# Optimization experiments

Hardware: AMD Instinct MI355X
Metric: run time of the kernel (lower is better)

## Reference

```python
import jax, jax.numpy as jnp
import numpy as np

N_NODES = 100000
N_EDGES = 1600000
D_FEAT = 32


def setup_inputs() -> dict:
    key = jax.random.key(0)
    k1, k2, k3, k4, k5 = jax.random.split(key, 5)
    src_feats = jax.random.normal(k1, (N_NODES, D_FEAT), dtype=jnp.float32)
    cj = jax.random.uniform(k2, (N_NODES, 1), dtype=jnp.float32)
    ci = jax.random.uniform(k3, (N_NODES, 1), dtype=jnp.float32)
    src_idx = jax.random.randint(k4, (N_EDGES,), 0, N_NODES, dtype=jnp.int32)
    dst_idx = jax.random.randint(k5, (N_EDGES,), 0, N_NODES, dtype=jnp.int32)
    return {"src_feats": src_feats, "cj": cj, "ci": ci,
            "src_idx": src_idx, "dst_idx": dst_idx}


def reference(src_feats, cj, ci, src_idx, dst_idx):
    # Dropout in eval mode (identity). Training-mode dropout is stochastic and
    # excluded from the correctness baseline.
    weighted = src_feats * cj                      # [N, d] scale by src norm coeff
    msgs = weighted[src_idx]                       # [E, d] gather (copy_u)
    agg = jax.ops.segment_sum(msgs, dst_idx, num_segments=N_NODES)  # [N, d] sum aggregate
    return agg * ci                                # [N, d] scale by dst norm coeff
```

## Files before the change

### kernel.cpp

```cpp
#include <hip/hip_runtime.h>
#include <hip/hip_fp16.h>

#define N_NODES 100000
#define N_EDGES 1600000
#define D_FEAT 32
#define CAP 32
#define NXCD 8
#define NODES_PER_XCD (N_NODES / NXCD)
#define EDGE_THREADS (N_EDGES / 4)
#define EDGE_BLOCKS ((EDGE_THREADS + 255) / 256)

typedef int   __attribute__((ext_vector_type(4))) i32x4;
typedef float __attribute__((ext_vector_type(4))) f32x4;

__global__ __launch_bounds__(256) void lgc_weight(
    const f32x4* __restrict__ feats4,
    const float* __restrict__ cj,
    __half2*     __restrict__ w2)
{
    int tid = blockIdx.x * 256 + threadIdx.x;
    float c = cj[tid >> 3];
    f32x4 v = __builtin_nontemporal_load(&feats4[tid]);
    __half2 h0 = __floats2half2_rn(v.x * c, v.y * c);
    __half2 h1 = __floats2half2_rn(v.z * c, v.w * c);
    w2[tid * 2 + 0] = h0;
    w2[tid * 2 + 1] = h1;
}

__global__ __launch_bounds__(256) void lgc_bucket(
    const i32x4*  __restrict__ dst4,
    const i32x4*  __restrict__ src4,
    const __half* __restrict__ weighted,
    int*          __restrict__ cnt,
    int*          __restrict__ bucket,
    float*        __restrict__ out)
{
    int x  = blockIdx.x % NXCD;
    int lb = blockIdx.x / NXCD;
    int t  = lb * 256 + threadIdx.x;
    if (t >= EDGE_THREADS) return;

    const int lo = x * NODES_PER_XCD;
    const int hi = lo + NODES_PER_XCD;

    i32x4 d4 = __builtin_nontemporal_load(&dst4[t]);
    bool ix = (d4.x >= lo) & (d4.x < hi);
    bool iy = (d4.y >= lo) & (d4.y < hi);
    bool iz = (d4.z >= lo) & (d4.z < hi);
    bool iw = (d4.w >= lo) & (d4.w < hi);
    if (!(ix | iy | iz | iw)) return;

    i32x4 s4 = __builtin_nontemporal_load(&src4[t]);
    int ds[4] = {d4.x, d4.y, d4.z, d4.w};
    int ss[4] = {s4.x, s4.y, s4.z, s4.w};
    bool in[4] = {ix, iy, iz, iw};

    #pragma unroll
    for (int k = 0; k < 4; ++k) {
        if (!in[k]) continue;
        int d = ds[k], s = ss[k];
        int pos = atomicAdd(&cnt[d], 1);
        if (pos < CAP) {
            bucket[(size_t)d * CAP + pos] = s;
        } else {
            const __half* row = weighted + (size_t)s * D_FEAT;
            float* o = out + (size_t)d * D_FEAT;
            for (int f = 0; f < D_FEAT; ++f)
                atomicAdd(o + f, __half2float(row[f]));
        }
    }
}

__global__ __launch_bounds__(256) void lgc_gather(
    const __half* __restrict__ w,
    const float*  __restrict__ ci,
    const int*    __restrict__ cnt,
    const i32x4*  __restrict__ bucket4,
    f32x4*        __restrict__ out4)
{
    int tid = blockIdx.x * 256 + threadIdx.x;
    if (tid >= N_NODES * 4) return;
    int n = tid >> 2;
    int q = tid & 3;

    int c = cnt[n];
    if (c > CAP) c = CAP;
    const i32x4* b4 = bucket4 + (size_t)n * (CAP / 4);

    i32x4 r[8];
    #pragma unroll
    for (int j = 0; j < 8; ++j)
        if (j * 4 < c) r[j] = __builtin_nontemporal_load(&b4[j]);

    float acc[8] = {0.f, 0.f, 0.f, 0.f, 0.f, 0.f, 0.f, 0.f};

    auto acc_row = [&](int s) {
        uint4 u = *reinterpret_cast<const uint4*>(w + (size_t)s * D_FEAT + q * 8);
        float2 f0 = __half22float2(*reinterpret_cast<__half2*>(&u.x));
        float2 f1 = __half22float2(*reinterpret_cast<__half2*>(&u.y));
        float2 f2 = __half22float2(*reinterpret_cast<__half2*>(&u.z));
        float2 f3 = __half22float2(*reinterpret_cast<__half2*>(&u.w));
        acc[0] += f0.x; acc[1] += f0.y; acc[2] += f1.x; acc[3] += f1.y;
        acc[4] += f2.x; acc[5] += f2.y; acc[6] += f3.x; acc[7] += f3.y;
    };

    #pragma unroll
    for (int j = 0; j < 8; ++j) {
        int base = j * 4;
        if (base < c) {
            i32x4 bv = r[j];
            acc_row(bv.x);
            if (base + 1 < c) acc_row(bv.y);
            if (base + 2 < c) acc_row(bv.z);
            if (base + 3 < c) acc_row(bv.w);
        }
    }

    float s = ci[n];
    size_t ob = (size_t)n * 8 + q * 2;
    f32x4 o0 = __builtin_nontemporal_load(&out4[ob]);
    f32x4 o1 = __builtin_nontemporal_load(&out4[ob + 1]);
    f32x4 a0 = {acc[0], acc[1], acc[2], acc[3]};
    f32x4 a1 = {acc[4], acc[5], acc[6], acc[7]};
    __builtin_nontemporal_store((a0 + o0) * s, &out4[ob]);
    __builtin_nontemporal_store((a1 + o1) * s, &out4[ob + 1]);
}

__global__ __launch_bounds__(256) void lgc_scatter(
    const float4* __restrict__ src_feats4,
    const float*  __restrict__ cj,
    const int*    __restrict__ src_idx,
    const int*    __restrict__ dst_idx,
    float*        __restrict__ out)
{
    long tid = (long)blockIdx.x * blockDim.x + threadIdx.x;
    const long total = (long)N_EDGES * 8;
    if (tid >= total) return;
    int e  = (int)(tid >> 3);
    int f4 = (int)(tid & 7);
    int s = src_idx[e];
    int d = dst_idx[e];
    float c = cj[s];
    float4 v = src_feats4[s * 8 + f4];
    float* o = out + (size_t)d * D_FEAT + f4 * 4;
    atomicAdd(o + 0, v.x * c);
    atomicAdd(o + 1, v.y * c);
    atomicAdd(o + 2, v.z * c);
    atomicAdd(o + 3, v.w * c);
}

__global__ __launch_bounds__(256) void lgc_scale(
    float4*       __restrict__ out4,
    const float*  __restrict__ ci)
{
    int tid = blockIdx.x * blockDim.x + threadIdx.x;
    const int total = N_NODES * 8;
    if (tid >= total) return;
    float c = ci[tid >> 3];
    float4 v = out4[tid];
    v.x *= c; v.y *= c; v.z *= c; v.w *= c;
    out4[tid] = v;
}

extern "C" void kernel_launch(void* const* d_in, const int* in_sizes, int n_in,
                              void* d_out, int out_size, void* d_ws, size_t ws_size,
                              hipStream_t stream) {
    const float* src_feats = (const float*)d_in[0];
    const float* cj        = (const float*)d_in[1];
    const float* ci        = (const float*)d_in[2];
    const int*   src_idx   = (const int*)d_in[3];
    const int*   dst_idx   = (const int*)d_in[4];
    float*       out       = (float*)d_out;

    const size_t cnt_ints    = 102400;
    const size_t bucket_ints = (size_t)N_NODES * CAP;
    const size_t wfeat_bytes = (size_t)N_NODES * D_FEAT * sizeof(__half);
    const size_t need = (cnt_ints + bucket_ints) * 4 + wfeat_bytes;

    if (ws_size >= need) {
        int*    cnt      = (int*)d_ws;
        int*    bucket   = cnt + cnt_ints;
        __half* weighted = (__half*)(bucket + bucket_ints);

        hipMemsetAsync(cnt, 0, N_NODES * sizeof(int), stream);
        hipMemsetAsync(out, 0, (size_t)out_size * sizeof(float), stream);

        lgc_weight<<<(N_NODES * 8) / 256, 256, 0, stream>>>(
            (const f32x4*)src_feats, cj, (__half2*)weighted);

        lgc_bucket<<<NXCD * EDGE_BLOCKS, 256, 0, stream>>>(
            (const i32x4*)dst_idx, (const i32x4*)src_idx, weighted,
            cnt, bucket, out);

        lgc_gather<<<(N_NODES * 4 + 255) / 256, 256, 0, stream>>>(
            weighted, ci, cnt, (const i32x4*)bucket, (f32x4*)out);
    } else {
        hipMemsetAsync(out, 0, (size_t)out_size * sizeof(float), stream);
        {
            const long total = (long)N_EDGES * 8;
            const int grid = (int)((total + 255) / 256);
            lgc_scatter<<<grid, 256, 0, stream>>>((const float4*)src_feats, cj,
                                                  src_idx, dst_idx, out);
        }
        {
            const int grid = (N_NODES * 8 + 255) / 256;
            lgc_scale<<<grid, 256, 0, stream>>>((float4*)out, ci);
        }
    }
}
```

Baseline: 176.1 us.

## Cut bucket passes to four and batch gather loads eight at a time

The bucketing kernel now splits destination nodes into four ranges instead of eight, so the edge index arrays are re-read fewer times, though each pass touches a wider slice of the counters. The gather kernel now issues up to eight row loads before accumulating any of them, which gives more memory-level parallelism per thread at the cost of extra registers. The spill path is moved into a helper function with no change in behaviour.

```diff
diff --git a/kernel.cpp b/kernel.cpp
--- a/kernel.cpp
+++ b/kernel.cpp
@@ -5,8 +5,8 @@
 #define N_EDGES 1600000
 #define D_FEAT 32
 #define CAP 32
-#define NXCD 8
-#define NODES_PER_XCD (N_NODES / NXCD)
+#define NPASS 4
+#define NODES_PER_P (N_NODES / NPASS)
 #define EDGE_THREADS (N_EDGES / 4)
 #define EDGE_BLOCKS ((EDGE_THREADS + 255) / 256)
 
@@ -21,10 +21,16 @@
     int tid = blockIdx.x * 256 + threadIdx.x;
     float c = cj[tid >> 3];
     f32x4 v = __builtin_nontemporal_load(&feats4[tid]);
-    __half2 h0 = __floats2half2_rn(v.x * c, v.y * c);
-    __half2 h1 = __floats2half2_rn(v.z * c, v.w * c);
-    w2[tid * 2 + 0] = h0;
-    w2[tid * 2 + 1] = h1;
+    w2[tid * 2 + 0] = __floats2half2_rn(v.x * c, v.y * c);
+    w2[tid * 2 + 1] = __floats2half2_rn(v.z * c, v.w * c);
+}
+
+__device__ __forceinline__ void spill_row(const __half* __restrict__ weighted,
+                                          float* __restrict__ out, int s, int d)
+{
+    const __half* row = weighted + (size_t)s * D_FEAT;
+    float* o = out + (size_t)d * D_FEAT;
+    for (int f = 0; f < D_FEAT; ++f) atomicAdd(o + f, __half2float(row[f]));
 }
 
 __global__ __launch_bounds__(256) void lgc_bucket(
@@ -35,13 +41,13 @@
     int*          __restrict__ bucket,
     float*        __restrict__ out)
 {
-    int x  = blockIdx.x % NXCD;
-    int lb = blockIdx.x / NXCD;
+    int x  = blockIdx.x % NPASS;
+    int lb = blockIdx.x / NPASS;
     int t  = lb * 256 + threadIdx.x;
     if (t >= EDGE_THREADS) return;
 
-    const int lo = x * NODES_PER_XCD;
-    const int hi = lo + NODES_PER_XCD;
+    const int lo = x * NODES_PER_P;
+    const int hi = lo + NODES_PER_P;
 
     i32x4 d4 = __builtin_nontemporal_load(&dst4[t]);
     bool ix = (d4.x >= lo) & (d4.x < hi);
@@ -63,20 +69,17 @@
         if (pos < CAP) {
             bucket[(size_t)d * CAP + pos] = s;
         } else {
-            const __half* row = weighted + (size_t)s * D_FEAT;
-            float* o = out + (size_t)d * D_FEAT;
-            for (int f = 0; f < D_FEAT; ++f)
-                atomicAdd(o + f, __half2float(row[f]));
+            spill_row(weighted, out, s, d);
         }
     }
 }
 
 __global__ __launch_bounds__(256) void lgc_gather(
-    const __half* __restrict__ w,
-    const float*  __restrict__ ci,
-    const int*    __restrict__ cnt,
-    const i32x4*  __restrict__ bucket4,
-    f32x4*        __restrict__ out4)
+    const uint4* __restrict__ w4,
+    const float* __restrict__ ci,
+    const int*   __restrict__ cnt,
+    const i32x4* __restrict__ bucket4,
+    f32x4*       __restrict__ out4)
 {
     int tid = blockIdx.x * 256 + threadIdx.x;
     if (tid >= N_NODES * 4) return;
@@ -94,36 +97,42 @@
 
     float acc[8] = {0.f, 0.f, 0.f, 0.f, 0.f, 0.f, 0.f, 0.f};
 
-    auto acc_row = [&](int s) {
-        uint4 u = *reinterpret_cast<const uint4*>(w + (size_t)s * D_FEAT + q * 8);
-        float2 f0 = __half22float2(*reinterpret_cast<__half2*>(&u.x));
-        float2 f1 = __half22float2(*reinterpret_cast<__half2*>(&u.y));
-        float2 f2 = __half22float2(*reinterpret_cast<__half2*>(&u.z));
-        float2 f3 = __half22float2(*reinterpret_cast<__half2*>(&u.w));
-        acc[0] += f0.x; acc[1] += f0.y; acc[2] += f1.x; acc[3] += f1.y;
-        acc[4] += f2.x; acc[5] += f2.y; acc[6] += f3.x; acc[7] += f3.y;
-    };
-
     #pragma unroll
-    for (int j = 0; j < 8; ++j) {
-        int base = j * 4;
+    for (int b = 0; b < 4; ++b) {
+        const int base = b * 8;
         if (base < c) {
-            i32x4 bv = r[j];
-            acc_row(bv.x);
-            if (base + 1 < c) acc_row(bv.y);
-            if (base + 2 < c) acc_row(bv.z);
-            if (base + 3 < c) acc_row(bv.w);
+            int m = c - base;
+            uint4 v[8];
+            #pragma unroll
+            for (int t = 0; t < 8; ++t) {
+                if (t < m) {
+                    int s = ((const int*)r)[base + t];
+                    v[t] = w4[(size_t)s * 4 + q];
+                }
+            }
+            #pragma unroll
+            for (int t = 0; t < 8; ++t) {
+                if (t < m) {
+                    unsigned ux = v[t].x, uy = v[t].y, uz = v[t].z, uw = v[t].w;
+                    float2 f0 = __half22float2(*(__half2*)&ux);
+                    float2 f1 = __half22float2(*(__half2*)&uy);
+                    float2 f2 = __half22float2(*(__half2*)&uz);
+                    float2 f3 = __half22float2(*(__half2*)&uw);
+                    acc[0] += f0.x; acc[1] += f0.y; acc[2] += f1.x; acc[3] += f1.y;
+                    acc[4] += f2.x; acc[5] += f2.y; acc[6] += f3.x; acc[7] += f3.y;
+                }
+            }
         }
     }
 
-    float s = ci[n];
+    float sc = ci[n];
     size_t ob = (size_t)n * 8 + q * 2;
     f32x4 o0 = __builtin_nontemporal_load(&out4[ob]);
     f32x4 o1 = __builtin_nontemporal_load(&out4[ob + 1]);
     f32x4 a0 = {acc[0], acc[1], acc[2], acc[3]};
     f32x4 a1 = {acc[4], acc[5], acc[6], acc[7]};
-    __builtin_nontemporal_store((a0 + o0) * s, &out4[ob]);
-    __builtin_nontemporal_store((a1 + o1) * s, &out4[ob + 1]);
+    __builtin_nontemporal_store((a0 + o0) * sc, &out4[ob]);
+    __builtin_nontemporal_store((a1 + o1) * sc, &out4[ob + 1]);
 }
 
 __global__ __launch_bounds__(256) void lgc_scatter(
@@ -188,12 +197,12 @@
         lgc_weight<<<(N_NODES * 8) / 256, 256, 0, stream>>>(
             (const f32x4*)src_feats, cj, (__half2*)weighted);
 
-        lgc_bucket<<<NXCD * EDGE_BLOCKS, 256, 0, stream>>>(
+        lgc_bucket<<<NPASS * EDGE_BLOCKS, 256, 0, stream>>>(
             (const i32x4*)dst_idx, (const i32x4*)src_idx, weighted,
             cnt, bucket, out);
 
         lgc_gather<<<(N_NODES * 4 + 255) / 256, 256, 0, stream>>>(
-            weighted, ci, cnt, (const i32x4*)bucket, (f32x4*)out);
+            (const uint4*)weighted, ci, cnt, (const i32x4*)bucket, (f32x4*)out);
     } else {
         hipMemsetAsync(out, 0, (size_t)out_size * sizeof(float), stream);
         {
```

Measured after the change: 180.3 us. 1.02x slower.
